# Performance work log

Hardware: AMD Instinct MI355X
Metric: run time of the kernel (lower is better)

The kernel has to match this reference:

```python
import jax, jax.numpy as jnp
import numpy as np

INDIM = 1024
OUTDIM = 1024
NNZ = 65536  # expander pattern: avg degree 64 per output row
N = 50000


def setup_inputs() -> dict:
    key = jax.random.key(0)
    k1, k2, k3, k4, k5 = jax.random.split(key, 5)
    x = jax.random.normal(k1, (N, INDIM), dtype=jnp.float32)
    # glorot init for nnz values as in reset_parameters('glorot')
    stdv = np.sqrt(6.0 / (INDIM + OUTDIM))
    nnz_weight = jax.random.uniform(k2, (NNZ,), dtype=jnp.float32, minval=-stdv, maxval=stdv)
    bias = jax.random.normal(k3, (OUTDIM,), dtype=jnp.float32) * 0.02
    row = jax.random.randint(k4, (NNZ,), 0, OUTDIM, dtype=jnp.int64)
    col = jax.random.randint(k5, (NNZ,), 0, INDIM, dtype=jnp.int64)
    edge_index = jnp.stack([row, col])  # [2, NNZ]
    return {"x": x, "nnz_weight": nnz_weight, "bias": bias, "edge_index": edge_index}


def reference(x, nnz_weight, bias, edge_index):
    # SparseTensor(row, col, sizes=(outdim, indim), value=nnz_weight);
    # y = (W @ x^T)^T + bias  ==  x @ W^T + bias
    # Sparsity pattern is fixed & small (1024x1024): scatter values into a
    # dense weight then use a dense GEMM (duplicates accumulate, matching SpMM).
    row, col = edge_index[0], edge_index[1]
    W = jnp.zeros((OUTDIM, INDIM), dtype=nnz_weight.dtype).at[row, col].add(nnz_weight)
    return x @ W.T + bias  # [N, OUTDIM]
```

## Files before the change

### kernel.cpp

```cpp
#include <hip/hip_runtime.h>
#include <cstdint>

#define INDIM 1024
#define OUTDIM 1024
#define NNZ 65536
#define M_ROWS 50000

typedef __bf16 bf16x8 __attribute__((ext_vector_type(8)));
typedef float f32x4 __attribute__((ext_vector_type(4)));
typedef unsigned int u32x4 __attribute__((ext_vector_type(4)));

__global__ void scatter_w_kernel(const float* __restrict__ vals,
                                 const int* __restrict__ edge,
                                 float* __restrict__ Wf) {
    int e = blockIdx.x * blockDim.x + threadIdx.x;
    if (e < NNZ) {
        int r = edge[e];
        int c = edge[NNZ + e];
        atomicAdd(&Wf[r * INDIM + c], vals[e]);
    }
}

__global__ void cvt_w_kernel(const float* __restrict__ Wf,
                             unsigned short* __restrict__ Wb) {
    int i = blockIdx.x * blockDim.x + threadIdx.x;
    unsigned u = __builtin_bit_cast(unsigned, Wf[i]) + 0x8000u;
    Wb[i] = (unsigned short)(u >> 16);
}

__device__ __forceinline__ unsigned pack_bf16x2(float a, float b) {
    unsigned ua = __builtin_bit_cast(unsigned, a) + 0x8000u;
    unsigned ub = __builtin_bit_cast(unsigned, b) + 0x8000u;
    return (ua >> 16) | (ub & 0xffff0000u);
}

__device__ __forceinline__ void async_copy16(const void* g, void* l) {
    __builtin_amdgcn_global_load_lds(
        (const __attribute__((address_space(1))) void*)g,
        (__attribute__((address_space(3))) void*)l, 16, 0, 0);
}

__global__ void __launch_bounds__(256)
gemm_bt_kernel(const float* __restrict__ X,
               const unsigned short* __restrict__ Wb,
               const float* __restrict__ bias,
               float* __restrict__ out) {
    __shared__ unsigned As[128 * 16];
    __shared__ unsigned short Bs[128 * 32];

    const int t = threadIdx.x;
    const int w = t >> 6;
    const int l = t & 63;
    const int wr = w >> 1;
    const int wc = w & 1;
    const int quad = l >> 4;
    const int lr = l & 15;
    const int m0 = blockIdx.y * 128;
    const int n0 = blockIdx.x * 128;

    const int ar  = t >> 1;
    const int akh = (t & 1) * 16;
    int arow = m0 + ar;
    if (arow >= M_ROWS) arow = M_ROWS - 1;
    const float* aptr = X + (long)arow * INDIM + akh;
    unsigned* as_dst = &As[ar * 16 + (akh >> 1)];

    f32x4 acc[4][4];
#pragma unroll
    for (int i = 0; i < 4; i++)
#pragma unroll
        for (int j = 0; j < 4; j++) acc[i][j] = (f32x4)0.0f;

    float biasv[4];
#pragma unroll
    for (int j = 0; j < 4; j++) biasv[j] = bias[n0 + wc * 64 + j * 16 + lr];

    for (int kt = 0; kt < INDIM; kt += 32) {
#pragma unroll
        for (int i = 0; i < 2; i++) {
            int c = i * 256 + t;
            int brow = c >> 2;
            int part = c & 3;
            const unsigned short* g = Wb + (long)(n0 + brow) * INDIM + kt + part * 8;
            char* lbase = (char*)Bs + (size_t)(i * 256 + w * 64) * 16;
            async_copy16(g, lbase);
        }

        const float* ap = aptr + kt;
        f32x4 f0 = *(const f32x4*)(ap);
        f32x4 f1 = *(const f32x4*)(ap + 4);
        f32x4 f2 = *(const f32x4*)(ap + 8);
        f32x4 f3 = *(const f32x4*)(ap + 12);
        u32x4 p0, p1;
        p0.x = pack_bf16x2(f0.x, f0.y);
        p0.y = pack_bf16x2(f0.z, f0.w);
        p0.z = pack_bf16x2(f1.x, f1.y);
        p0.w = pack_bf16x2(f1.z, f1.w);
        p1.x = pack_bf16x2(f2.x, f2.y);
        p1.y = pack_bf16x2(f2.z, f2.w);
        p1.z = pack_bf16x2(f3.x, f3.y);
        p1.w = pack_bf16x2(f3.z, f3.w);
        *(u32x4*)(as_dst)     = p0;
        *(u32x4*)(as_dst + 4) = p1;

        __syncthreads();

        bf16x8 af[4], bf[4];
#pragma unroll
        for (int i = 0; i < 4; i++) {
            int row = wr * 64 + i * 16 + lr;
            af[i] = *(const bf16x8*)((const unsigned short*)As + row * 32 + quad * 8);
        }
#pragma unroll
        for (int j = 0; j < 4; j++) {
            int row = wc * 64 + j * 16 + lr;
            bf[j] = *(const bf16x8*)(Bs + row * 32 + quad * 8);
        }
#pragma unroll
        for (int i = 0; i < 4; i++)
#pragma unroll
            for (int j = 0; j < 4; j++)
                acc[i][j] = __builtin_amdgcn_mfma_f32_16x16x32_bf16(af[i], bf[j], acc[i][j], 0, 0, 0);

        __syncthreads();
    }

#pragma unroll
    for (int i = 0; i < 4; i++) {
#pragma unroll
        for (int j = 0; j < 4; j++) {
            int col = n0 + wc * 64 + j * 16 + lr;
#pragma unroll
            for (int r = 0; r < 4; r++) {
                int row = m0 + wr * 64 + i * 16 + quad * 4 + r;
                if (row < M_ROWS) {
                    out[(long)row * OUTDIM + col] = acc[i][j][r] + biasv[j];
                }
            }
        }
    }
}

extern "C" void kernel_launch(void* const* d_in, const int* in_sizes, int n_in,
                              void* d_out, int out_size, void* d_ws, size_t ws_size,
                              hipStream_t stream) {
    const float* x    = (const float*)d_in[0];
    const float* nnzw = (const float*)d_in[1];
    const float* bias = (const float*)d_in[2];
    const int* edge   = (const int*)d_in[3];
    float* out        = (float*)d_out;

    float* Wf         = (float*)d_ws;
    unsigned short* Wb = (unsigned short*)((char*)d_ws + (size_t)OUTDIM * INDIM * 4);

    hipMemsetAsync(Wf, 0, (size_t)OUTDIM * INDIM * sizeof(float), stream);

    scatter_w_kernel<<<NNZ / 256, 256, 0, stream>>>(nnzw, edge, Wf);
    cvt_w_kernel<<<(OUTDIM * INDIM) / 256, 256, 0, stream>>>(Wf, Wb);

    dim3 grid(OUTDIM / 128, (M_ROWS + 127) / 128);
    gemm_bt_kernel<<<grid, 256, 0, stream>>>(x, Wb, bias, out);
}
```

Measured before the change: 545.3 us.

## XOR-swizzle LDS tiles and remap block order for grouped L2 reuse

Applies an XOR swizzle to the 16-byte chunk positions in the A and B shared-memory tiles, on both the write side and the MFMA fragment reads, to reduce LDS bank conflicts. It also replaces the 2D grid with a 1D grid of 3128 blocks and remaps block IDs so groups of 8 M-tiles sweep all 8 N-tiles together, with a tail for the remaining M-tiles. The remap is meant to improve L2/MALL reuse of X rows across N-tiles. The hardcoded block counts tie the kernel to fixed problem sizes.

```diff
diff --git a/kernel.cpp b/kernel.cpp
--- a/kernel.cpp
+++ b/kernel.cpp
@@ -55,15 +55,29 @@
     const int wc = w & 1;
     const int quad = l >> 4;
     const int lr = l & 15;
-    const int m0 = blockIdx.y * 128;
-    const int n0 = blockIdx.x * 128;
+
+    const int bid = blockIdx.x;
+    int m_t, n_t;
+    if (bid < 3072) {
+        m_t = ((bid >> 6) << 3) + (bid & 7);
+        n_t = (bid >> 3) & 7;
+    } else {
+        int r = bid - 3072;
+        m_t = 384 + (r >> 3);
+        n_t = r & 7;
+    }
+    const int m0 = m_t * 128;
+    const int n0 = n_t * 128;
 
     const int ar  = t >> 1;
-    const int akh = (t & 1) * 16;
+    const int ac0 = (t & 1) * 2;
+    const int as_sw = (ar >> 1) & 3;
     int arow = m0 + ar;
     if (arow >= M_ROWS) arow = M_ROWS - 1;
-    const float* aptr = X + (long)arow * INDIM + akh;
-    unsigned* as_dst = &As[ar * 16 + (akh >> 1)];
+    const float* aptr = X + (long)arow * INDIM + (t & 1) * 16;
+    unsigned* as_row = &As[ar * 16];
+    const int aph0 = (ac0 ^ as_sw) * 4;
+    const int aph1 = ((ac0 + 1) ^ as_sw) * 4;
 
     f32x4 acc[4][4];
 #pragma unroll
@@ -75,13 +89,22 @@
 #pragma unroll
     for (int j = 0; j < 4; j++) biasv[j] = bias[n0 + wc * 64 + j * 16 + lr];
 
+    int bsrc_off[2];
+    int brow_[2];
+#pragma unroll
+    for (int i = 0; i < 2; i++) {
+        int c_idx = i * 256 + t;
+        int brow = c_idx >> 2;
+        int pphys = c_idx & 3;
+        int pdata = pphys ^ ((brow >> 1) & 3);
+        brow_[i] = brow;
+        bsrc_off[i] = pdata * 8;
+    }
+
     for (int kt = 0; kt < INDIM; kt += 32) {
 #pragma unroll
         for (int i = 0; i < 2; i++) {
-            int c = i * 256 + t;
-            int brow = c >> 2;
-            int part = c & 3;
-            const unsigned short* g = Wb + (long)(n0 + brow) * INDIM + kt + part * 8;
+            const unsigned short* g = Wb + (long)(n0 + brow_[i]) * INDIM + kt + bsrc_off[i];
             char* lbase = (char*)Bs + (size_t)(i * 256 + w * 64) * 16;
             async_copy16(g, lbase);
         }
@@ -100,8 +123,8 @@
         p1.y = pack_bf16x2(f2.z, f2.w);
         p1.z = pack_bf16x2(f3.x, f3.y);
         p1.w = pack_bf16x2(f3.z, f3.w);
-        *(u32x4*)(as_dst)     = p0;
-        *(u32x4*)(as_dst + 4) = p1;
+        *(u32x4*)(as_row + aph0) = p0;
+        *(u32x4*)(as_row + aph1) = p1;
 
         __syncthreads();
 
@@ -109,12 +132,14 @@
 #pragma unroll
         for (int i = 0; i < 4; i++) {
             int row = wr * 64 + i * 16 + lr;
-            af[i] = *(const bf16x8*)((const unsigned short*)As + row * 32 + quad * 8);
+            int ph = quad ^ ((row >> 1) & 3);
+            af[i] = *(const bf16x8*)((const unsigned short*)As + row * 32 + ph * 8);
         }
 #pragma unroll
         for (int j = 0; j < 4; j++) {
             int row = wc * 64 + j * 16 + lr;
-            bf[j] = *(const bf16x8*)(Bs + row * 32 + quad * 8);
+            int ph = quad ^ ((row >> 1) & 3);
+            bf[j] = *(const bf16x8*)(Bs + row * 32 + ph * 8);
         }
 #pragma unroll
         for (int i = 0; i < 4; i++)
@@ -158,6 +183,5 @@
     scatter_w_kernel<<<NNZ / 256, 256, 0, stream>>>(nnzw, edge, Wf);
     cvt_w_kernel<<<(OUTDIM * INDIM) / 256, 256, 0, stream>>>(Wf, Wb);
 
-    dim3 grid(OUTDIM / 128, (M_ROWS + 127) / 128);
-    gemm_bt_kernel<<<grid, 256, 0, stream>>>(x, Wb, bias, out);
+    gemm_bt_kernel<<<dim3(3128), 256, 0, stream>>>(x, Wb, bias, out);
 }
```

New measurement: 519.3 us. 1.05x faster.
